# Optimization experiments

Measured on AMD Instinct MI355X. Metric: run time of the kernel, lower is better.

The kernel has to match this reference:

```python
import jax, jax.numpy as jnp
import numpy as np

B, N, DIN, H, DOUT = 32, 1024, 256, 256, 256
NEG = 9000000000000000.0  # -9e15 masking trick from the original code


def setup_inputs() -> dict:
    key = jax.random.key(0)
    ks = jax.random.split(key, 10)
    x = jax.random.normal(ks[0], (B, N, DIN), dtype=jnp.float32)
    # binary float mask (1 = edge present)
    mask = jax.random.randint(ks[1], (B, N, N), 0, 2).astype(jnp.float32)
    s = 0.02
    Wv = jax.random.normal(ks[2], (DIN, H), dtype=jnp.float32) * s
    bv = jnp.zeros((H,), jnp.float32)
    Wk = jax.random.normal(ks[3], (DIN, H), dtype=jnp.float32) * s
    bk = jnp.zeros((H,), jnp.float32)
    Wq = jax.random.normal(ks[4], (DIN, H), dtype=jnp.float32) * s
    bq = jnp.zeros((H,), jnp.float32)
    Wo = jax.random.normal(ks[5], (H, DOUT), dtype=jnp.float32) * s
    bo = jnp.zeros((DOUT,), jnp.float32)
    return {"x": x, "mask": mask, "Wv": Wv, "bv": bv, "Wk": Wk, "bk": bk,
            "Wq": Wq, "bq": bq, "Wo": Wo, "bo": bo}


def reference(x, mask, Wv, bv, Wk, bk, Wq, bq, Wo, bo):
    # x: [B,N,din], mask: [B,N,N]
    v = jax.nn.relu(x @ Wv + bv)              # [B,N,H]
    q = jax.nn.relu(x @ Wq + bq)              # [B,N,H]
    k = jax.nn.relu(x @ Wk + bk)              # [B,N,H]
    scores = jnp.einsum('bnh,bmh->bnm', q, k)  # QK^T, [B,N,N]
    att = jax.nn.softmax(scores * mask - NEG * (1.0 - mask), axis=-1)
    out = jnp.einsum('bnm,bmh->bnh', att, v)   # AV
    return jax.nn.relu(out @ Wo + bo)          # [B,N,d_out]
```

## Files before the change

### kernel.cpp

```cpp
#include <hip/hip_runtime.h>


typedef __attribute__((ext_vector_type(4))) float    f32x4;
typedef __attribute__((ext_vector_type(8))) short    s16x8;
typedef __attribute__((ext_vector_type(4))) short    s16x4;
typedef unsigned long long u64;

__device__ __forceinline__ short f2b(float f) {
    union { float f; unsigned u; } v; v.f = f;
    unsigned r = v.u + 0x7FFFu + ((v.u >> 16) & 1u);
    return (short)(r >> 16);
}

__device__ __forceinline__ void gl_lds16(const short* g, short* l) {
    __builtin_amdgcn_global_load_lds(
        (const __attribute__((address_space(1))) unsigned int*)g,
        (__attribute__((address_space(3))) unsigned int*)l, 16, 0, 0);
}

__global__ void prep_w(const float* __restrict__ Wq, const float* __restrict__ Wk,
                       const float* __restrict__ Wv, const float* __restrict__ Wo,
                       short* __restrict__ Wt) {
    int idx = blockIdx.x * 256 + threadIdx.x;
    int w = idx >> 16, rem = idx & 65535;
    int n = rem >> 8, kk = rem & 255;
    const float* W = (w == 0) ? Wq : (w == 1) ? Wk : (w == 2) ? Wv : Wo;
    Wt[idx] = f2b(W[kk * 256 + n]);
}

__global__ __launch_bounds__(256) void qkv_gemm(
        const float* __restrict__ x, const short* __restrict__ Wt,
        const float* __restrict__ bq, const float* __restrict__ bk, const float* __restrict__ bv,
        short* __restrict__ qO, short* __restrict__ kO, short* __restrict__ vtO) {
    __shared__ short a_lds[128][72];
    __shared__ short b_lds[3][64][72];
    const int tid = threadIdx.x;
    const int bm = blockIdx.x >> 2, bn = blockIdx.x & 3;
    const int s0 = bm * 128, n0 = bn * 64;
    const int wid = tid >> 6, l = tid & 63, lo4 = l & 15, hi4 = l >> 4;
    const int wm = wid >> 1, wn = wid & 1;

    f32x4 acc[3][4][2];
    #pragma unroll
    for (int w = 0; w < 3; ++w)
        #pragma unroll
        for (int mi = 0; mi < 4; ++mi)
            #pragma unroll
            for (int ni = 0; ni < 2; ++ni)
                acc[w][mi][ni] = (f32x4){0.f, 0.f, 0.f, 0.f};

    for (int kt = 0; kt < 4; ++kt) {
        const int k0 = kt * 64;
        #pragma unroll
        for (int i = 0; i < 8; ++i) {
            int ch = i * 256 + tid;
            int row = ch >> 4, c4 = (ch & 15) * 4;
            f32x4 xv = *(const f32x4*)(x + (size_t)(s0 + row) * 256 + k0 + c4);
            s16x4 pk = { f2b(xv.x), f2b(xv.y), f2b(xv.z), f2b(xv.w) };
            *(s16x4*)&a_lds[row][c4] = pk;
        }
        #pragma unroll
        for (int w = 0; w < 3; ++w) {
            #pragma unroll
            for (int i = 0; i < 2; ++i) {
                int ch = i * 256 + tid;
                int n = ch >> 3, c8 = (ch & 7) * 8;
                *(s16x8*)&b_lds[w][n][c8] =
                    *(const s16x8*)(Wt + (size_t)w * 65536 + (size_t)(n0 + n) * 256 + k0 + c8);
            }
        }
        __syncthreads();
        s16x8 af[4][2];
        #pragma unroll
        for (int mi = 0; mi < 4; ++mi)
            #pragma unroll
            for (int kk = 0; kk < 2; ++kk)
                af[mi][kk] = *(s16x8*)&a_lds[wm * 64 + mi * 16 + lo4][kk * 32 + hi4 * 8];
        #pragma unroll
        for (int w = 0; w < 3; ++w)
            #pragma unroll
            for (int ni = 0; ni < 2; ++ni)
                #pragma unroll
                for (int kk = 0; kk < 2; ++kk) {
                    s16x8 bfr = *(s16x8*)&b_lds[w][wn * 32 + ni * 16 + lo4][kk * 32 + hi4 * 8];
                    #pragma unroll
                    for (int mi = 0; mi < 4; ++mi)
                        acc[w][mi][ni] = __builtin_amdgcn_mfma_f32_16x16x32_bf16(
                            af[mi][kk], bfr, acc[w][mi][ni], 0, 0, 0);
                }
        __syncthreads();
    }

    const float* bias[3] = { bq, bk, bv };
    for (int w = 0; w < 3; ++w) {
        #pragma unroll
        for (int mi = 0; mi < 4; ++mi)
            #pragma unroll
            for (int ni = 0; ni < 2; ++ni)
                #pragma unroll
                for (int j = 0; j < 4; ++j) {
                    int r = wm * 64 + mi * 16 + hi4 * 4 + j;
                    int c = wn * 32 + ni * 16 + lo4;
                    float v = acc[w][mi][ni][j] + bias[w][n0 + c];
                    a_lds[r][c] = f2b(fmaxf(v, 0.f));
                }
        __syncthreads();
        if (w == 0) {
            #pragma unroll
            for (int i = 0; i < 4; ++i) {
                int ch = i * 256 + tid;
                int row = ch >> 3, c8 = (ch & 7) * 8;
                *(s16x8*)(qO + (size_t)(s0 + row) * 256 + n0 + c8) = *(s16x8*)&a_lds[row][c8];
            }
        } else if (w == 1) {
            #pragma unroll
            for (int i = 0; i < 4; ++i) {
                int ch = i * 256 + tid;
                int row = ch >> 3, c8 = (ch & 7) * 8;
                int swz = ((c8 >> 3) ^ (row & 7)) * 8;
                *(s16x8*)(kO + (size_t)(s0 + row) * 256 + n0 + swz) = *(s16x8*)&a_lds[row][c8];
            }
        } else {
            int bb = s0 >> 10, nn = s0 & 1023;
            #pragma unroll
            for (int i = 0; i < 4; ++i) {
                int ch = i * 256 + tid;
                int h = ch >> 4, sc = (ch & 15) * 8;
                s16x8 t;
                #pragma unroll
                for (int e = 0; e < 8; ++e) t[e] = a_lds[sc + e][h];
                int cil = sc >> 3;
                int swz = (cil & 8) | ((cil & 7) ^ ((n0 + h) & 7));
                *(s16x8*)(vtO + ((size_t)bb * 256 + n0 + h) * 1024 + nn + swz * 8) = t;
            }
        }
        __syncthreads();
    }
}

__global__ __launch_bounds__(512) void attn(
        const short* __restrict__ q, const short* __restrict__ k,
        const short* __restrict__ vt, const float* __restrict__ mask,
        short* __restrict__ attv) {
    __shared__ short kbuf[2][16384];
    __shared__ short vbuf[2][16384];
    __shared__ short p_lds[8][16][72];
    const int tid = threadIdx.x, wid = tid >> 6, l = tid & 63;
    const int lo4 = l & 15, hi4 = l >> 4;
    const int bid = blockIdx.x;
    const int swz = (bid & 7) * 32 + (bid >> 3);
    const int b = swz >> 3, qb = swz & 7;
    const int q0 = qb * 128 + wid * 16;
    const size_t bq_row = (size_t)b * 1024 + q0;

    const short* kb  = k  + (size_t)b * 1024 * 256;
    const short* vtg = vt + (size_t)b * 256 * 1024;
    const float* mtb = mask + ((size_t)b * 1024 + q0) * 1024;

#define STAGE_K(bufi, c0_) do { const short* sg_ = kb + (size_t)(c0_) * 256;          \
    _Pragma("unroll") for (int i_ = 0; i_ < 4; ++i_) { int cb_ = i_ * 512 + wid * 64; \
        gl_lds16(sg_ + (size_t)(cb_ + l) * 8, &kbuf[bufi][cb_ * 8]); } } while (0)
#define STAGE_V(bufi, c0_) do {                                                       \
    _Pragma("unroll") for (int i_ = 0; i_ < 4; ++i_) { int cb_ = i_ * 512 + wid * 64; \
        int ch_ = cb_ + l; int h_ = ch_ >> 3, cc_ = ch_ & 7;                          \
        gl_lds16(vtg + (size_t)h_ * 1024 + (c0_) + cc_ * 8, &vbuf[bufi][cb_ * 8]); } } while (0)
#define LOAD_MASK(dst, c0_) do {                                                      \
    _Pragma("unroll") for (int i_ = 0; i_ < 4; ++i_)                                  \
        dst[i_] = *(const f32x4*)(mtb + (size_t)(i_ * 4 + hi4) * 1024 + (c0_) + lo4 * 4); } while (0)

    s16x8 qf[8];
    {
        const short* qp = q + (bq_row + lo4) * 256 + hi4 * 8;
        #pragma unroll
        for (int t = 0; t < 8; ++t) qf[t] = *(const s16x8*)(qp + t * 32);
    }
    f32x4 oacc[16];
    #pragma unroll
    for (int t = 0; t < 16; ++t) oacc[t] = (f32x4){0.f, 0.f, 0.f, 0.f};
    float m_run[4] = { -1e30f, -1e30f, -1e30f, -1e30f };
    float l_run[4] = { 0.f, 0.f, 0.f, 0.f };
    f32x4 mkc[4], mkn[4];

    STAGE_K(0, 0);
    LOAD_MASK(mkc, 0);
    STAGE_V(0, 0);

    for (int t = 0; t < 16; ++t) {
        const int cur = t & 1;
        const int c0 = t * 64;
        if (t < 15) {
            STAGE_K(cur ^ 1, c0 + 64);
            LOAD_MASK(mkn, c0 + 64);
            asm volatile("s_waitcnt vmcnt(16)" ::: "memory");
        } else {
            asm volatile("s_waitcnt vmcnt(8)" ::: "memory");
        }
        __builtin_amdgcn_s_barrier();
        f32x4 s[4];
        #pragma unroll
        for (int ct = 0; ct < 4; ++ct) s[ct] = (f32x4){0.f, 0.f, 0.f, 0.f};
        __builtin_amdgcn_s_setprio(1);
        #pragma unroll
        for (int ct = 0; ct < 4; ++ct) {
            int row = ct * 16 + lo4, rx = row & 7;
            #pragma unroll
            for (int tt = 0; tt < 8; ++tt) {
                int ch = tt * 4 + hi4;
                int sc = (ch & 24) | ((ch & 7) ^ rx);
                s16x8 kf = *(s16x8*)&kbuf[cur][row * 256 + sc * 8];
                s[ct] = __builtin_amdgcn_mfma_f32_16x16x32_bf16(qf[tt], kf, s[ct], 0, 0, 0);
            }
        }
        __builtin_amdgcn_s_setprio(0);
        u64 bw[4][4];
        #pragma unroll
        for (int i = 0; i < 4; ++i) {
            bw[i][0] = __ballot(mkc[i].x != 0.f);
            bw[i][1] = __ballot(mkc[i].y != 0.f);
            bw[i][2] = __ballot(mkc[i].z != 0.f);
            bw[i][3] = __ballot(mkc[i].w != 0.f);
        }
        const int cc = lo4 & 3;
        u64 w0 = (cc == 0) ? bw[0][0] : (cc == 1) ? bw[0][1] : (cc == 2) ? bw[0][2] : bw[0][3];
        u64 w1 = (cc == 0) ? bw[1][0] : (cc == 1) ? bw[1][1] : (cc == 2) ? bw[1][2] : bw[1][3];
        u64 w2 = (cc == 0) ? bw[2][0] : (cc == 1) ? bw[2][1] : (cc == 2) ? bw[2][2] : bw[2][3];
        u64 w3 = (cc == 0) ? bw[3][0] : (cc == 1) ? bw[3][1] : (cc == 2) ? bw[3][2] : bw[3][3];
        u64 wsel = (hi4 == 0) ? w0 : (hi4 == 1) ? w1 : (hi4 == 2) ? w2 : w3;
        const unsigned sh0 = (unsigned)(lo4 >> 2);
        float sm[4][4];
        #pragma unroll
        for (int j = 0; j < 4; ++j) {
            unsigned wsx = (unsigned)(wsel >> (j * 16 + sh0));
            sm[0][j] = (wsx & 1u)    ? s[0][j] : -1e30f;
            sm[1][j] = (wsx & 16u)   ? s[1][j] : -1e30f;
            sm[2][j] = (wsx & 256u)  ? s[2][j] : -1e30f;
            sm[3][j] = (wsx & 4096u) ? s[3][j] : -1e30f;
        }
        float scale[4], p[4][4];
        #pragma unroll
        for (int j = 0; j < 4; ++j) {
            float tmx = fmaxf(fmaxf(sm[0][j], sm[1][j]), fmaxf(sm[2][j], sm[3][j]));
            tmx = fmaxf(tmx, __shfl_xor(tmx, 1));
            tmx = fmaxf(tmx, __shfl_xor(tmx, 2));
            tmx = fmaxf(tmx, __shfl_xor(tmx, 4));
            tmx = fmaxf(tmx, __shfl_xor(tmx, 8));
            float mnew = fmaxf(m_run[j], tmx);
            scale[j] = __expf(m_run[j] - mnew);
            m_run[j] = mnew;
            float su = 0.f;
            #pragma unroll
            for (int ct = 0; ct < 4; ++ct) { p[ct][j] = __expf(sm[ct][j] - mnew); su += p[ct][j]; }
            su += __shfl_xor(su, 1);
            su += __shfl_xor(su, 2);
            su += __shfl_xor(su, 4);
            su += __shfl_xor(su, 8);
            l_run[j] = l_run[j] * scale[j] + su;
        }
        #pragma unroll
        for (int tt = 0; tt < 16; ++tt)
            #pragma unroll
            for (int j = 0; j < 4; ++j) oacc[tt][j] *= scale[j];
        #pragma unroll
        for (int ct = 0; ct < 4; ++ct)
            #pragma unroll
            for (int j = 0; j < 4; ++j)
                p_lds[wid][hi4 * 4 + j][ct * 16 + lo4] = f2b(p[ct][j]);
        asm volatile("s_waitcnt lgkmcnt(0)" ::: "memory");
        __builtin_amdgcn_sched_barrier(0);
        s16x8 pa0 = *(s16x8*)&p_lds[wid][lo4][hi4 * 8];
        s16x8 pa1 = *(s16x8*)&p_lds[wid][lo4][32 + hi4 * 8];
        if (t < 15) {
            STAGE_V(cur ^ 1, c0 + 64);
            asm volatile("s_waitcnt vmcnt(12)" ::: "memory");
        } else {
            asm volatile("s_waitcnt vmcnt(0)" ::: "memory");
        }
        __builtin_amdgcn_s_barrier();
        __builtin_amdgcn_s_setprio(1);
        #pragma unroll
        for (int nt = 0; nt < 16; ++nt) {
            int h = nt * 16 + lo4, hx = h & 7;
            s16x8 vf0 = *(s16x8*)&vbuf[cur][h * 64 + (hi4 ^ hx) * 8];
            s16x8 vf1 = *(s16x8*)&vbuf[cur][h * 64 + ((hi4 + 4) ^ hx) * 8];
            oacc[nt] = __builtin_amdgcn_mfma_f32_16x16x32_bf16(pa0, vf0, oacc[nt], 0, 0, 0);
            oacc[nt] = __builtin_amdgcn_mfma_f32_16x16x32_bf16(pa1, vf1, oacc[nt], 0, 0, 0);
        }
        __builtin_amdgcn_s_setprio(0);
        if (t < 15) {
            #pragma unroll
            for (int i = 0; i < 4; ++i) mkc[i] = mkn[i];
        }
    }
    float inv[4];
    #pragma unroll
    for (int j = 0; j < 4; ++j) inv[j] = 1.f / l_run[j];
    #pragma unroll
    for (int g = 0; g < 4; ++g) {
        asm volatile("s_waitcnt lgkmcnt(0)" ::: "memory");
        #pragma unroll
        for (int ntl = 0; ntl < 4; ++ntl)
            #pragma unroll
            for (int j = 0; j < 4; ++j)
                p_lds[wid][hi4 * 4 + j][ntl * 16 + lo4] = f2b(oacc[g * 4 + ntl][j] * inv[j]);
        asm volatile("s_waitcnt lgkmcnt(0)" ::: "memory");
        __builtin_amdgcn_sched_barrier(0);
        s16x8 r0 = *(s16x8*)&p_lds[wid][lo4][hi4 * 16];
        s16x8 r1 = *(s16x8*)&p_lds[wid][lo4][hi4 * 16 + 8];
        short* op = attv + (bq_row + lo4) * 256 + g * 64 + hi4 * 16;
        *(s16x8*)op = r0;
        *(s16x8*)(op + 8) = r1;
    }
#undef STAGE_K
#undef STAGE_V
#undef LOAD_MASK
}

__global__ __launch_bounds__(256) void out_gemm(
        const short* __restrict__ a, const short* __restrict__ Wto,
        const float* __restrict__ bo, float* __restrict__ out) {
    __shared__ short a_lds[128][72];
    __shared__ short b_lds[64][72];
    __shared__ float bounce[128][68];
    const int tid = threadIdx.x;
    const int bm = blockIdx.x >> 2, bn = blockIdx.x & 3;
    const int s0 = bm * 128, n0 = bn * 64;
    const int wid = tid >> 6, l = tid & 63, lo4 = l & 15, hi4 = l >> 4;
    const int wm = wid >> 1, wn = wid & 1;
    f32x4 acc[4][2];
    #pragma unroll
    for (int mi = 0; mi < 4; ++mi)
        #pragma unroll
        for (int ni = 0; ni < 2; ++ni) acc[mi][ni] = (f32x4){0.f, 0.f, 0.f, 0.f};

    for (int kt = 0; kt < 4; ++kt) {
        const int k0 = kt * 64;
        #pragma unroll
        for (int i = 0; i < 4; ++i) {
            int ch = i * 256 + tid;
            int row = ch >> 3, c8 = (ch & 7) * 8;
            *(s16x8*)&a_lds[row][c8] = *(const s16x8*)(a + (size_t)(s0 + row) * 256 + k0 + c8);
        }
        #pragma unroll
        for (int i = 0; i < 2; ++i) {
            int ch = i * 256 + tid;
            int n = ch >> 3, c8 = (ch & 7) * 8;
            *(s16x8*)&b_lds[n][c8] = *(const s16x8*)(Wto + (size_t)(n0 + n) * 256 + k0 + c8);
        }
        __syncthreads();
        s16x8 af[4][2];
        #pragma unroll
        for (int mi = 0; mi < 4; ++mi)
            #pragma unroll
            for (int kk = 0; kk < 2; ++kk)
                af[mi][kk] = *(s16x8*)&a_lds[wm * 64 + mi * 16 + lo4][kk * 32 + hi4 * 8];
        #pragma unroll
        for (int ni = 0; ni < 2; ++ni)
            #pragma unroll
            for (int kk = 0; kk < 2; ++kk) {
                s16x8 bfr = *(s16x8*)&b_lds[wn * 32 + ni * 16 + lo4][kk * 32 + hi4 * 8];
                #pragma unroll
                for (int mi = 0; mi < 4; ++mi)
                    acc[mi][ni] = __builtin_amdgcn_mfma_f32_16x16x32_bf16(
                        af[mi][kk], bfr, acc[mi][ni], 0, 0, 0);
            }
        __syncthreads();
    }
    #pragma unroll
    for (int mi = 0; mi < 4; ++mi)
        #pragma unroll
        for (int ni = 0; ni < 2; ++ni)
            #pragma unroll
            for (int j = 0; j < 4; ++j) {
                int r = wm * 64 + mi * 16 + hi4 * 4 + j;
                int c = wn * 32 + ni * 16 + lo4;
                bounce[r][c] = fmaxf(acc[mi][ni][j] + bo[n0 + c], 0.f);
            }
    __syncthreads();
    #pragma unroll
    for (int i = 0; i < 8; ++i) {
        int ch = i * 256 + tid;
        int row = ch >> 4, c4 = (ch & 15) * 4;
        *(f32x4*)(out + (size_t)(s0 + row) * 256 + n0 + c4) = *(f32x4*)&bounce[row][c4];
    }
}

extern "C" void kernel_launch(void* const* d_in, const int* in_sizes, int n_in,
                              void* d_out, int out_size, void* d_ws, size_t ws_size,
                              hipStream_t stream) {
    const float* x    = (const float*)d_in[0];
    const float* mask = (const float*)d_in[1];
    const float* Wv   = (const float*)d_in[2];
    const float* bv   = (const float*)d_in[3];
    const float* Wk   = (const float*)d_in[4];
    const float* bk   = (const float*)d_in[5];
    const float* Wq   = (const float*)d_in[6];
    const float* bq   = (const float*)d_in[7];
    const float* Wo   = (const float*)d_in[8];
    const float* bo   = (const float*)d_in[9];
    float* out = (float*)d_out;

    char* ws = (char*)d_ws;
    short* Wt   = (short*)ws;
    short* qB   = (short*)(ws + (1 << 20));
    short* kB   = qB  + (size_t)32768 * 256;
    short* vtB  = kB  + (size_t)32768 * 256;
    short* avB  = vtB + (size_t)32768 * 256;
    (void)in_sizes; (void)n_in; (void)out_size; (void)ws_size;

    prep_w<<<1024, 256, 0, stream>>>(Wq, Wk, Wv, Wo, Wt);
    qkv_gemm<<<1024, 256, 0, stream>>>(x, Wt, bq, bk, bv, qB, kB, vtB);
    attn<<<256, 512, 0, stream>>>(qB, kB, vtB, mask, avB);
    out_gemm<<<1024, 256, 0, stream>>>(avB, Wt + 3 * 65536, bo, out);
}
```

Before: 139.2 us.

## Preload mask as LDS bitmasks and reuse V buffer for P staging

Each wave now loads its whole 16x1024 float mask slice up front, packs it into 64-bit ballot bitmasks and stores them in LDS. The main loop then reads four u64 words per tile instead of issuing per-tile global mask loads and ballots. The P-tile staging area moves into the idle half of the V double buffer with an XOR swizzle, and the next V stage is issued after the barrier so it can overlap the PV MFMAs. This front-loads a burst of mask loads before the loop and changes the vmcnt accounting and buffer-reuse ordering, which raises hazard risk.

```diff
diff --git a/kernel.cpp b/kernel.cpp
--- a/kernel.cpp
+++ b/kernel.cpp
@@ -144,7 +144,7 @@
         short* __restrict__ attv) {
     __shared__ short kbuf[2][16384];
     __shared__ short vbuf[2][16384];
-    __shared__ short p_lds[8][16][72];
+    __shared__ u64 mask_lds[2048];
     const int tid = threadIdx.x, wid = tid >> 6, l = tid & 63;
     const int lo4 = l & 15, hi4 = l >> 4;
     const int bid = blockIdx.x;
@@ -155,7 +155,6 @@
 
     const short* kb  = k  + (size_t)b * 1024 * 256;
     const short* vtg = vt + (size_t)b * 256 * 1024;
-    const float* mtb = mask + ((size_t)b * 1024 + q0) * 1024;
 
 #define STAGE_K(bufi, c0_) do { const short* sg_ = kb + (size_t)(c0_) * 256;          \
     _Pragma("unroll") for (int i_ = 0; i_ < 4; ++i_) { int cb_ = i_ * 512 + wid * 64; \
@@ -164,9 +163,9 @@
     _Pragma("unroll") for (int i_ = 0; i_ < 4; ++i_) { int cb_ = i_ * 512 + wid * 64; \
         int ch_ = cb_ + l; int h_ = ch_ >> 3, cc_ = ch_ & 7;                          \
         gl_lds16(vtg + (size_t)h_ * 1024 + (c0_) + cc_ * 8, &vbuf[bufi][cb_ * 8]); } } while (0)
-#define LOAD_MASK(dst, c0_) do {                                                      \
-    _Pragma("unroll") for (int i_ = 0; i_ < 4; ++i_)                                  \
-        dst[i_] = *(const f32x4*)(mtb + (size_t)(i_ * 4 + hi4) * 1024 + (c0_) + lo4 * 4); } while (0)
+
+    STAGE_K(0, 0);
+    STAGE_V(0, 0);
 
     s16x8 qf[8];
     {
@@ -174,26 +173,47 @@
         #pragma unroll
         for (int t = 0; t < 8; ++t) qf[t] = *(const s16x8*)(qp + t * 32);
     }
+
+    {
+        const float* mrow = mask + bq_row * 1024 + l * 4;
+        #pragma unroll
+        for (int g = 0; g < 8; ++g) {
+            f32x4 va[8];
+            #pragma unroll
+            for (int i = 0; i < 8; ++i) {
+                int u = g * 8 + i, rr = u >> 2, ch = u & 3;
+                va[i] = *(const f32x4*)(mrow + (size_t)rr * 1024 + ch * 256);
+            }
+            #pragma unroll
+            for (int i = 0; i < 8; ++i) {
+                int u = g * 8 + i, rr = u >> 2, ch = u & 3;
+                u64 b0 = __ballot(va[i].x != 0.f);
+                u64 b1 = __ballot(va[i].y != 0.f);
+                u64 b2 = __ballot(va[i].z != 0.f);
+                u64 b3 = __ballot(va[i].w != 0.f);
+                if (l < 4) {
+                    u64 bb = (l == 0) ? b0 : (l == 1) ? b1 : (l == 2) ? b2 : b3;
+                    mask_lds[(wid * 16 + rr) * 16 + ch * 4 + l] = bb;
+                }
+            }
+        }
+    }
+
     f32x4 oacc[16];
     #pragma unroll
     for (int t = 0; t < 16; ++t) oacc[t] = (f32x4){0.f, 0.f, 0.f, 0.f};
     float m_run[4] = { -1e30f, -1e30f, -1e30f, -1e30f };
     float l_run[4] = { 0.f, 0.f, 0.f, 0.f };
-    f32x4 mkc[4], mkn[4];
-
-    STAGE_K(0, 0);
-    LOAD_MASK(mkc, 0);
-    STAGE_V(0, 0);
+    const int swp = (lo4 & 7) * 8;
 
     for (int t = 0; t < 16; ++t) {
         const int cur = t & 1;
         const int c0 = t * 64;
         if (t < 15) {
             STAGE_K(cur ^ 1, c0 + 64);
-            LOAD_MASK(mkn, c0 + 64);
-            asm volatile("s_waitcnt vmcnt(16)" ::: "memory");
+            asm volatile("s_waitcnt vmcnt(4)" ::: "memory");
         } else {
-            asm volatile("s_waitcnt vmcnt(8)" ::: "memory");
+            asm volatile("s_waitcnt vmcnt(0)" ::: "memory");
         }
         __builtin_amdgcn_s_barrier();
         f32x4 s[4];
@@ -212,25 +232,15 @@
             }
         }
         __builtin_amdgcn_s_setprio(0);
-        u64 bw[4][4];
-        #pragma unroll
-        for (int i = 0; i < 4; ++i) {
-            bw[i][0] = __ballot(mkc[i].x != 0.f);
-            bw[i][1] = __ballot(mkc[i].y != 0.f);
-            bw[i][2] = __ballot(mkc[i].z != 0.f);
-            bw[i][3] = __ballot(mkc[i].w != 0.f);
-        }
-        const int cc = lo4 & 3;
-        u64 w0 = (cc == 0) ? bw[0][0] : (cc == 1) ? bw[0][1] : (cc == 2) ? bw[0][2] : bw[0][3];
-        u64 w1 = (cc == 0) ? bw[1][0] : (cc == 1) ? bw[1][1] : (cc == 2) ? bw[1][2] : bw[1][3];
-        u64 w2 = (cc == 0) ? bw[2][0] : (cc == 1) ? bw[2][1] : (cc == 2) ? bw[2][2] : bw[2][3];
-        u64 w3 = (cc == 0) ? bw[3][0] : (cc == 1) ? bw[3][1] : (cc == 2) ? bw[3][2] : bw[3][3];
-        u64 wsel = (hi4 == 0) ? w0 : (hi4 == 1) ? w1 : (hi4 == 2) ? w2 : w3;
-        const unsigned sh0 = (unsigned)(lo4 >> 2);
+        u64 mkc[4];
+        #pragma unroll
+        for (int j = 0; j < 4; ++j)
+            mkc[j] = mask_lds[(wid * 16 + hi4 * 4 + j) * 16 + (t >> 2) * 4 + (lo4 & 3)];
+        const unsigned shx = ((unsigned)(t & 3) << 4) | (unsigned)(lo4 >> 2);
         float sm[4][4];
         #pragma unroll
         for (int j = 0; j < 4; ++j) {
-            unsigned wsx = (unsigned)(wsel >> (j * 16 + sh0));
+            unsigned wsx = (unsigned)(mkc[j] >> shx);
             sm[0][j] = (wsx & 1u)    ? s[0][j] : -1e30f;
             sm[1][j] = (wsx & 16u)   ? s[1][j] : -1e30f;
             sm[2][j] = (wsx & 256u)  ? s[2][j] : -1e30f;
@@ -260,22 +270,21 @@
         for (int tt = 0; tt < 16; ++tt)
             #pragma unroll
             for (int j = 0; j < 4; ++j) oacc[tt][j] *= scale[j];
+        short* pb = &vbuf[cur ^ 1][wid * 1024];
         #pragma unroll
         for (int ct = 0; ct < 4; ++ct)
             #pragma unroll
-            for (int j = 0; j < 4; ++j)
-                p_lds[wid][hi4 * 4 + j][ct * 16 + lo4] = f2b(p[ct][j]);
+            for (int j = 0; j < 4; ++j) {
+                int r = hi4 * 4 + j;
+                pb[r * 64 + ((ct * 16 + lo4) ^ ((r & 7) * 8))] = f2b(p[ct][j]);
+            }
         asm volatile("s_waitcnt lgkmcnt(0)" ::: "memory");
         __builtin_amdgcn_sched_barrier(0);
-        s16x8 pa0 = *(s16x8*)&p_lds[wid][lo4][hi4 * 8];
-        s16x8 pa1 = *(s16x8*)&p_lds[wid][lo4][32 + hi4 * 8];
-        if (t < 15) {
-            STAGE_V(cur ^ 1, c0 + 64);
-            asm volatile("s_waitcnt vmcnt(12)" ::: "memory");
-        } else {
-            asm volatile("s_waitcnt vmcnt(0)" ::: "memory");
-        }
+        s16x8 pa0 = *(s16x8*)&pb[lo4 * 64 + ((hi4 * 8) ^ swp)];
+        s16x8 pa1 = *(s16x8*)&pb[lo4 * 64 + ((32 + hi4 * 8) ^ swp)];
+        asm volatile("s_waitcnt lgkmcnt(0)" ::: "memory");
         __builtin_amdgcn_s_barrier();
+        if (t < 15) STAGE_V(cur ^ 1, c0 + 64);
         __builtin_amdgcn_s_setprio(1);
         #pragma unroll
         for (int nt = 0; nt < 16; ++nt) {
@@ -286,33 +295,31 @@
             oacc[nt] = __builtin_amdgcn_mfma_f32_16x16x32_bf16(pa1, vf1, oacc[nt], 0, 0, 0);
         }
         __builtin_amdgcn_s_setprio(0);
-        if (t < 15) {
-            #pragma unroll
-            for (int i = 0; i < 4; ++i) mkc[i] = mkn[i];
-        }
     }
     float inv[4];
     #pragma unroll
     for (int j = 0; j < 4; ++j) inv[j] = 1.f / l_run[j];
+    short* pbE = &vbuf[0][wid * 1024];
     #pragma unroll
     for (int g = 0; g < 4; ++g) {
         asm volatile("s_waitcnt lgkmcnt(0)" ::: "memory");
         #pragma unroll
         for (int ntl = 0; ntl < 4; ++ntl)
             #pragma unroll
-            for (int j = 0; j < 4; ++j)
-                p_lds[wid][hi4 * 4 + j][ntl * 16 + lo4] = f2b(oacc[g * 4 + ntl][j] * inv[j]);
+            for (int j = 0; j < 4; ++j) {
+                int r = hi4 * 4 + j;
+                pbE[r * 64 + ((ntl * 16 + lo4) ^ ((r & 7) * 8))] = f2b(oacc[g * 4 + ntl][j] * inv[j]);
+            }
         asm volatile("s_waitcnt lgkmcnt(0)" ::: "memory");
         __builtin_amdgcn_sched_barrier(0);
-        s16x8 r0 = *(s16x8*)&p_lds[wid][lo4][hi4 * 16];
-        s16x8 r1 = *(s16x8*)&p_lds[wid][lo4][hi4 * 16 + 8];
+        s16x8 r0 = *(s16x8*)&pbE[lo4 * 64 + ((hi4 * 16) ^ swp)];
+        s16x8 r1 = *(s16x8*)&pbE[lo4 * 64 + ((hi4 * 16 + 8) ^ swp)];
         short* op = attv + (bq_row + lo4) * 256 + g * 64 + hi4 * 16;
         *(s16x8*)op = r0;
         *(s16x8*)(op + 8) = r1;
     }
 #undef STAGE_K
 #undef STAGE_V
-#undef LOAD_MASK
 }
 
 __global__ __launch_bounds__(256) void out_gemm(
```

Result: slower. 150.7 us (+8.3%).

## Add producer warps that pack mask into bitmasks in LDS for attention

Applied to the files above, without the earlier changes.

The attention kernel grows from 8 to 12 waves. The four extra producer waves load the float mask tiles one step ahead, turn them into 64-bit ballot bitmasks and write those into a double-buffered LDS array. The compute waves now read a single u64 per lane instead of loading the mask and running ballots, with vmcnt waits retuned to match. This takes mask load traffic and ballot work off the MFMA waves, but producers and consumers must now match barrier counts, and the larger block may reduce occupancy.

```diff
diff --git a/kernel.cpp b/kernel.cpp
--- a/kernel.cpp
+++ b/kernel.cpp
@@ -138,24 +138,52 @@
     }
 }
 
-__global__ __launch_bounds__(512) void attn(
+__global__ __launch_bounds__(768) void attn(
         const short* __restrict__ q, const short* __restrict__ k,
         const short* __restrict__ vt, const float* __restrict__ mask,
         short* __restrict__ attv) {
     __shared__ short kbuf[2][16384];
     __shared__ short vbuf[2][16384];
     __shared__ short p_lds[8][16][72];
+    __shared__ u64 B_lds[2][32][4];
     const int tid = threadIdx.x, wid = tid >> 6, l = tid & 63;
     const int lo4 = l & 15, hi4 = l >> 4;
     const int bid = blockIdx.x;
     const int swz = (bid & 7) * 32 + (bid >> 3);
     const int b = swz >> 3, qb = swz & 7;
+    const size_t bq0 = (size_t)b * 1024 + qb * 128;
+
+    if (wid >= 8) {
+        const int pw = wid - 8;
+        const float* mb = mask + (bq0 + pw * 32 + (l >> 4)) * 1024 + (l & 15) * 4;
+#define PACK(bufi, c0_) do {                                                   \
+        f32x4 va_[8];                                                          \
+        _Pragma("unroll") for (int i_ = 0; i_ < 8; ++i_)                       \
+            va_[i_] = *(const f32x4*)(mb + (size_t)i_ * 4096 + (c0_));         \
+        _Pragma("unroll") for (int i_ = 0; i_ < 8; ++i_) {                     \
+            u64 b0_ = __ballot(va_[i_].x != 0.f);                              \
+            u64 b1_ = __ballot(va_[i_].y != 0.f);                              \
+            u64 b2_ = __ballot(va_[i_].z != 0.f);                              \
+            u64 b3_ = __ballot(va_[i_].w != 0.f);                              \
+            if (l < 4) {                                                       \
+                u64 w_ = (l == 0) ? b0_ : (l == 1) ? b1_ : (l == 2) ? b2_ : b3_; \
+                B_lds[bufi][pw * 8 + i_][l] = w_;                              \
+            } } } while (0)
+        PACK(0, 0);
+        for (int t = 0; t < 16; ++t) {
+            if (t < 15) PACK((t + 1) & 1, (t + 1) * 64);
+            asm volatile("s_waitcnt lgkmcnt(0)" ::: "memory");
+            __builtin_amdgcn_s_barrier();
+            __builtin_amdgcn_s_barrier();
+        }
+#undef PACK
+        return;
+    }
+
     const int q0 = qb * 128 + wid * 16;
     const size_t bq_row = (size_t)b * 1024 + q0;
-
     const short* kb  = k  + (size_t)b * 1024 * 256;
     const short* vtg = vt + (size_t)b * 256 * 1024;
-    const float* mtb = mask + ((size_t)b * 1024 + q0) * 1024;
 
 #define STAGE_K(bufi, c0_) do { const short* sg_ = kb + (size_t)(c0_) * 256;          \
     _Pragma("unroll") for (int i_ = 0; i_ < 4; ++i_) { int cb_ = i_ * 512 + wid * 64; \
@@ -164,9 +192,6 @@
     _Pragma("unroll") for (int i_ = 0; i_ < 4; ++i_) { int cb_ = i_ * 512 + wid * 64; \
         int ch_ = cb_ + l; int h_ = ch_ >> 3, cc_ = ch_ & 7;                          \
         gl_lds16(vtg + (size_t)h_ * 1024 + (c0_) + cc_ * 8, &vbuf[bufi][cb_ * 8]); } } while (0)
-#define LOAD_MASK(dst, c0_) do {                                                      \
-    _Pragma("unroll") for (int i_ = 0; i_ < 4; ++i_)                                  \
-        dst[i_] = *(const f32x4*)(mtb + (size_t)(i_ * 4 + hi4) * 1024 + (c0_) + lo4 * 4); } while (0)
 
     s16x8 qf[8];
     {
@@ -174,26 +199,23 @@
         #pragma unroll
         for (int t = 0; t < 8; ++t) qf[t] = *(const s16x8*)(qp + t * 32);
     }
+    STAGE_K(0, 0);
+    STAGE_V(0, 0);
+
     f32x4 oacc[16];
     #pragma unroll
     for (int t = 0; t < 16; ++t) oacc[t] = (f32x4){0.f, 0.f, 0.f, 0.f};
     float m_run[4] = { -1e30f, -1e30f, -1e30f, -1e30f };
     float l_run[4] = { 0.f, 0.f, 0.f, 0.f };
-    f32x4 mkc[4], mkn[4];
-
-    STAGE_K(0, 0);
-    LOAD_MASK(mkc, 0);
-    STAGE_V(0, 0);
 
     for (int t = 0; t < 16; ++t) {
         const int cur = t & 1;
         const int c0 = t * 64;
         if (t < 15) {
             STAGE_K(cur ^ 1, c0 + 64);
-            LOAD_MASK(mkn, c0 + 64);
-            asm volatile("s_waitcnt vmcnt(16)" ::: "memory");
+            asm volatile("s_waitcnt vmcnt(8)" ::: "memory");
         } else {
-            asm volatile("s_waitcnt vmcnt(8)" ::: "memory");
+            asm volatile("s_waitcnt vmcnt(4)" ::: "memory");
         }
         __builtin_amdgcn_s_barrier();
         f32x4 s[4];
@@ -212,25 +234,12 @@
             }
         }
         __builtin_amdgcn_s_setprio(0);
-        u64 bw[4][4];
-        #pragma unroll
-        for (int i = 0; i < 4; ++i) {
-            bw[i][0] = __ballot(mkc[i].x != 0.f);
-            bw[i][1] = __ballot(mkc[i].y != 0.f);
-            bw[i][2] = __ballot(mkc[i].z != 0.f);
-            bw[i][3] = __ballot(mkc[i].w != 0.f);
-        }
-        const int cc = lo4 & 3;
-        u64 w0 = (cc == 0) ? bw[0][0] : (cc == 1) ? bw[0][1] : (cc == 2) ? bw[0][2] : bw[0][3];
-        u64 w1 = (cc == 0) ? bw[1][0] : (cc == 1) ? bw[1][1] : (cc == 2) ? bw[1][2] : bw[1][3];
-        u64 w2 = (cc == 0) ? bw[2][0] : (cc == 1) ? bw[2][1] : (cc == 2) ? bw[2][2] : bw[2][3];
-        u64 w3 = (cc == 0) ? bw[3][0] : (cc == 1) ? bw[3][1] : (cc == 2) ? bw[3][2] : bw[3][3];
-        u64 wsel = (hi4 == 0) ? w0 : (hi4 == 1) ? w1 : (hi4 == 2) ? w2 : w3;
+        u64 mk = B_lds[t & 1][wid * 4 + hi4][lo4 & 3];
         const unsigned sh0 = (unsigned)(lo4 >> 2);
         float sm[4][4];
         #pragma unroll
         for (int j = 0; j < 4; ++j) {
-            unsigned wsx = (unsigned)(wsel >> (j * 16 + sh0));
+            unsigned wsx = (unsigned)(mk >> (j * 16 + sh0));
             sm[0][j] = (wsx & 1u)    ? s[0][j] : -1e30f;
             sm[1][j] = (wsx & 16u)   ? s[1][j] : -1e30f;
             sm[2][j] = (wsx & 256u)  ? s[2][j] : -1e30f;
@@ -271,7 +280,7 @@
         s16x8 pa1 = *(s16x8*)&p_lds[wid][lo4][32 + hi4 * 8];
         if (t < 15) {
             STAGE_V(cur ^ 1, c0 + 64);
-            asm volatile("s_waitcnt vmcnt(12)" ::: "memory");
+            asm volatile("s_waitcnt vmcnt(8)" ::: "memory");
         } else {
             asm volatile("s_waitcnt vmcnt(0)" ::: "memory");
         }
@@ -286,10 +295,6 @@
             oacc[nt] = __builtin_amdgcn_mfma_f32_16x16x32_bf16(pa1, vf1, oacc[nt], 0, 0, 0);
         }
         __builtin_amdgcn_s_setprio(0);
-        if (t < 15) {
-            #pragma unroll
-            for (int i = 0; i < 4; ++i) mkc[i] = mkn[i];
-        }
     }
     float inv[4];
     #pragma unroll
@@ -312,7 +317,6 @@
     }
 #undef STAGE_K
 #undef STAGE_V
-#undef LOAD_MASK
 }
 
 __global__ __launch_bounds__(256) void out_gemm(
@@ -409,6 +413,6 @@
 
     prep_w<<<1024, 256, 0, stream>>>(Wq, Wk, Wv, Wo, Wt);
     qkv_gemm<<<1024, 256, 0, stream>>>(x, Wt, bq, bk, bv, qB, kB, vtB);
-    attn<<<256, 512, 0, stream>>>(qB, kB, vtB, mask, avB);
+    attn<<<256, 768, 0, stream>>>(qB, kB, vtB, mask, avB);
     out_gemm<<<1024, 256, 0, stream>>>(avB, Wt + 3 * 65536, bo, out);
 }
```

Result: slower. 147.9 us (+6.3%).

## Fuse output projection GEMM into attention kernel epilogue

Applied to the files above, without the earlier changes.

The attention kernel now keeps its normalized bf16 output tile in shared memory and multiplies it by Wo directly, applying bias and ReLU and writing the final fp32 output. This removes the separate out_gemm launch and the global round trip of the attention output. In exchange, each attention block stages Wo in four 64-column chunks with extra barriers, and the output stores are scalar and less coalesced.

```diff
diff --git a/kernel.cpp b/kernel.cpp
--- a/kernel.cpp
+++ b/kernel.cpp
@@ -138,12 +138,12 @@
     }
 }
 
-__global__ __launch_bounds__(512) void attn(
+__global__ __launch_bounds__(512) void attn_fused(
         const short* __restrict__ q, const short* __restrict__ k,
         const short* __restrict__ vt, const float* __restrict__ mask,
-        short* __restrict__ attv) {
-    __shared__ short kbuf[2][16384];
-    __shared__ short vbuf[2][16384];
+        const short* __restrict__ WtO, const float* __restrict__ bo,
+        float* __restrict__ out) {
+    __shared__ short SM[65536];
     __shared__ short p_lds[8][16][72];
     const int tid = threadIdx.x, wid = tid >> 6, l = tid & 63;
     const int lo4 = l & 15, hi4 = l >> 4;
@@ -151,19 +151,22 @@
     const int swz = (bid & 7) * 32 + (bid >> 3);
     const int b = swz >> 3, qb = swz & 7;
     const int q0 = qb * 128 + wid * 16;
+    const size_t bq0 = (size_t)b * 1024 + qb * 128;
     const size_t bq_row = (size_t)b * 1024 + q0;
 
     const short* kb  = k  + (size_t)b * 1024 * 256;
     const short* vtg = vt + (size_t)b * 256 * 1024;
-    const float* mtb = mask + ((size_t)b * 1024 + q0) * 1024;
-
+    const float* mtb = mask + bq_row * 1024;
+
+#define KBUF(bufi) (SM + (bufi) * 16384)
+#define VBUF(bufi) (SM + 32768 + (bufi) * 16384)
 #define STAGE_K(bufi, c0_) do { const short* sg_ = kb + (size_t)(c0_) * 256;          \
     _Pragma("unroll") for (int i_ = 0; i_ < 4; ++i_) { int cb_ = i_ * 512 + wid * 64; \
-        gl_lds16(sg_ + (size_t)(cb_ + l) * 8, &kbuf[bufi][cb_ * 8]); } } while (0)
+        gl_lds16(sg_ + (size_t)(cb_ + l) * 8, KBUF(bufi) + cb_ * 8); } } while (0)
 #define STAGE_V(bufi, c0_) do {                                                       \
     _Pragma("unroll") for (int i_ = 0; i_ < 4; ++i_) { int cb_ = i_ * 512 + wid * 64; \
         int ch_ = cb_ + l; int h_ = ch_ >> 3, cc_ = ch_ & 7;                          \
-        gl_lds16(vtg + (size_t)h_ * 1024 + (c0_) + cc_ * 8, &vbuf[bufi][cb_ * 8]); } } while (0)
+        gl_lds16(vtg + (size_t)h_ * 1024 + (c0_) + cc_ * 8, VBUF(bufi) + cb_ * 8); } } while (0)
 #define LOAD_MASK(dst, c0_) do {                                                      \
     _Pragma("unroll") for (int i_ = 0; i_ < 4; ++i_)                                  \
         dst[i_] = *(const f32x4*)(mtb + (size_t)(i_ * 4 + hi4) * 1024 + (c0_) + lo4 * 4); } while (0)
@@ -207,7 +210,7 @@
             for (int tt = 0; tt < 8; ++tt) {
                 int ch = tt * 4 + hi4;
                 int sc = (ch & 24) | ((ch & 7) ^ rx);
-                s16x8 kf = *(s16x8*)&kbuf[cur][row * 256 + sc * 8];
+                s16x8 kf = *(s16x8*)(KBUF(cur) + row * 256 + sc * 8);
                 s[ct] = __builtin_amdgcn_mfma_f32_16x16x32_bf16(qf[tt], kf, s[ct], 0, 0, 0);
             }
         }
@@ -280,8 +283,8 @@
         #pragma unroll
         for (int nt = 0; nt < 16; ++nt) {
             int h = nt * 16 + lo4, hx = h & 7;
-            s16x8 vf0 = *(s16x8*)&vbuf[cur][h * 64 + (hi4 ^ hx) * 8];
-            s16x8 vf1 = *(s16x8*)&vbuf[cur][h * 64 + ((hi4 + 4) ^ hx) * 8];
+            s16x8 vf0 = *(s16x8*)(VBUF(cur) + h * 64 + (hi4 ^ hx) * 8);
+            s16x8 vf1 = *(s16x8*)(VBUF(cur) + h * 64 + ((hi4 + 4) ^ hx) * 8);
             oacc[nt] = __builtin_amdgcn_mfma_f32_16x16x32_bf16(pa0, vf0, oacc[nt], 0, 0, 0);
             oacc[nt] = __builtin_amdgcn_mfma_f32_16x16x32_bf16(pa1, vf1, oacc[nt], 0, 0, 0);
         }
@@ -291,6 +294,8 @@
             for (int i = 0; i < 4; ++i) mkc[i] = mkn[i];
         }
     }
+    __syncthreads();
+
     float inv[4];
     #pragma unroll
     for (int j = 0; j < 4; ++j) inv[j] = 1.f / l_run[j];
@@ -306,82 +311,59 @@
         __builtin_amdgcn_sched_barrier(0);
         s16x8 r0 = *(s16x8*)&p_lds[wid][lo4][hi4 * 16];
         s16x8 r1 = *(s16x8*)&p_lds[wid][lo4][hi4 * 16 + 8];
-        short* op = attv + (bq_row + lo4) * 256 + g * 64 + hi4 * 16;
-        *(s16x8*)op = r0;
-        *(s16x8*)(op + 8) = r1;
-    }
+        int arow = wid * 16 + lo4;
+        *(s16x8*)&SM[arow * 264 + g * 64 + hi4 * 16]     = r0;
+        *(s16x8*)&SM[arow * 264 + g * 64 + hi4 * 16 + 8] = r1;
+    }
+    short* wo = SM + 33792;
+    #pragma unroll
+    for (int i = 0; i < 4; ++i) {
+        int idx = i * 512 + tid;
+        int n = idx >> 5, c8 = (idx & 31) * 8;
+        *(s16x8*)&wo[n * 264 + c8] = *(const s16x8*)(WtO + (size_t)n * 256 + c8);
+    }
+    __syncthreads();
+
+    for (int chk = 0; chk < 4; ++chk) {
+        const int n0 = chk * 64;
+        f32x4 acc2[4];
+        #pragma unroll
+        for (int ni = 0; ni < 4; ++ni) acc2[ni] = (f32x4){0.f, 0.f, 0.f, 0.f};
+        #pragma unroll
+        for (int kk = 0; kk < 8; ++kk) {
+            s16x8 af = *(s16x8*)&SM[(wid * 16 + lo4) * 264 + kk * 32 + hi4 * 8];
+            #pragma unroll
+            for (int ni = 0; ni < 4; ++ni) {
+                s16x8 bf = *(s16x8*)&wo[(ni * 16 + lo4) * 264 + kk * 32 + hi4 * 8];
+                acc2[ni] = __builtin_amdgcn_mfma_f32_16x16x32_bf16(af, bf, acc2[ni], 0, 0, 0);
+            }
+        }
+        #pragma unroll
+        for (int ni = 0; ni < 4; ++ni) {
+            float bv = bo[n0 + ni * 16 + lo4];
+            #pragma unroll
+            for (int j = 0; j < 4; ++j) {
+                int r = wid * 16 + hi4 * 4 + j;
+                out[(bq0 + r) * 256 + n0 + ni * 16 + lo4] = fmaxf(acc2[ni][j] + bv, 0.f);
+            }
+        }
+        if (chk < 3) {
+            __syncthreads();
+            #pragma unroll
+            for (int i = 0; i < 4; ++i) {
+                int idx = i * 512 + tid;
+                int n = idx >> 5, c8 = (idx & 31) * 8;
+                *(s16x8*)&wo[n * 264 + c8] =
+                    *(const s16x8*)(WtO + (size_t)(n0 + 64 + n) * 256 + c8);
+            }
+            __syncthreads();
+        }
+    }
+#undef KBUF
+#undef VBUF
 #undef STAGE_K
 #undef STAGE_V
 #undef LOAD_MASK
-}
-
-__global__ __launch_bounds__(256) void out_gemm(
-        const short* __restrict__ a, const short* __restrict__ Wto,
-        const float* __restrict__ bo, float* __restrict__ out) {
-    __shared__ short a_lds[128][72];
-    __shared__ short b_lds[64][72];
-    __shared__ float bounce[128][68];
-    const int tid = threadIdx.x;
-    const int bm = blockIdx.x >> 2, bn = blockIdx.x & 3;
-    const int s0 = bm * 128, n0 = bn * 64;
-    const int wid = tid >> 6, l = tid & 63, lo4 = l & 15, hi4 = l >> 4;
-    const int wm = wid >> 1, wn = wid & 1;
-    f32x4 acc[4][2];
-    #pragma unroll
-    for (int mi = 0; mi < 4; ++mi)
-        #pragma unroll
-        for (int ni = 0; ni < 2; ++ni) acc[mi][ni] = (f32x4){0.f, 0.f, 0.f, 0.f};
-
-    for (int kt = 0; kt < 4; ++kt) {
-        const int k0 = kt * 64;
-        #pragma unroll
-        for (int i = 0; i < 4; ++i) {
-            int ch = i * 256 + tid;
-            int row = ch >> 3, c8 = (ch & 7) * 8;
-            *(s16x8*)&a_lds[row][c8] = *(const s16x8*)(a + (size_t)(s0 + row) * 256 + k0 + c8);
-        }
-        #pragma unroll
-        for (int i = 0; i < 2; ++i) {
-            int ch = i * 256 + tid;
-            int n = ch >> 3, c8 = (ch & 7) * 8;
-            *(s16x8*)&b_lds[n][c8] = *(const s16x8*)(Wto + (size_t)(n0 + n) * 256 + k0 + c8);
-        }
-        __syncthreads();
-        s16x8 af[4][2];
-        #pragma unroll
-        for (int mi = 0; mi < 4; ++mi)
-            #pragma unroll
-            for (int kk = 0; kk < 2; ++kk)
-                af[mi][kk] = *(s16x8*)&a_lds[wm * 64 + mi * 16 + lo4][kk * 32 + hi4 * 8];
-        #pragma unroll
-        for (int ni = 0; ni < 2; ++ni)
-            #pragma unroll
-            for (int kk = 0; kk < 2; ++kk) {
-                s16x8 bfr = *(s16x8*)&b_lds[wn * 32 + ni * 16 + lo4][kk * 32 + hi4 * 8];
-                #pragma unroll
-                for (int mi = 0; mi < 4; ++mi)
-                    acc[mi][ni] = __builtin_amdgcn_mfma_f32_16x16x32_bf16(
-                        af[mi][kk], bfr, acc[mi][ni], 0, 0, 0);
-            }
-        __syncthreads();
-    }
-    #pragma unroll
-    for (int mi = 0; mi < 4; ++mi)
-        #pragma unroll
-        for (int ni = 0; ni < 2; ++ni)
-            #pragma unroll
-            for (int j = 0; j < 4; ++j) {
-                int r = wm * 64 + mi * 16 + hi4 * 4 + j;
-                int c = wn * 32 + ni * 16 + lo4;
-                bounce[r][c] = fmaxf(acc[mi][ni][j] + bo[n0 + c], 0.f);
-            }
-    __syncthreads();
-    #pragma unroll
-    for (int i = 0; i < 8; ++i) {
-        int ch = i * 256 + tid;
-        int row = ch >> 4, c4 = (ch & 15) * 4;
-        *(f32x4*)(out + (size_t)(s0 + row) * 256 + n0 + c4) = *(f32x4*)&bounce[row][c4];
-    }
 }
 
 extern "C" void kernel_launch(void* const* d_in, const int* in_sizes, int n_in,
@@ -404,11 +386,9 @@
     short* qB   = (short*)(ws + (1 << 20));
     short* kB   = qB  + (size_t)32768 * 256;
     short* vtB  = kB  + (size_t)32768 * 256;
-    short* avB  = vtB + (size_t)32768 * 256;
     (void)in_sizes; (void)n_in; (void)out_size; (void)ws_size;
 
     prep_w<<<1024, 256, 0, stream>>>(Wq, Wk, Wv, Wo, Wt);
     qkv_gemm<<<1024, 256, 0, stream>>>(x, Wt, bq, bk, bv, qB, kB, vtB);
-    attn<<<256, 512, 0, stream>>>(qB, kB, vtB, mask, avB);
-    out_gemm<<<1024, 256, 0, stream>>>(avB, Wt + 3 * 65536, bo, out);
-}
+    attn_fused<<<256, 512, 0, stream>>>(qB, kB, vtB, mask, Wt + 3 * 65536, bo, out);
+}
```

After: 123.8 us, median of 2. 1.12x faster.
